# Performance work log

Hardware: AMD Instinct MI355X
Metric: run time of the kernel (lower is better)

The kernel has to match this reference:

```python
import jax, jax.numpy as jnp
import numpy as np

N_NODES = 100000
N_EDGES = 1600000
IN_FEATS, HID_FEATS, OUT_FEATS = 64, 64, 32


def setup_inputs() -> dict:
    key = jax.random.key(0)
    ks = jax.random.split(key, 8)
    x = jax.random.normal(ks[0], (N_NODES, IN_FEATS), dtype=jnp.float32)
    edge_index = jax.random.randint(ks[1], (2, N_EDGES), 0, N_NODES, dtype=jnp.int64)
    s1 = 1.0 / np.sqrt(IN_FEATS)
    s2 = 1.0 / np.sqrt(HID_FEATS)
    return {
        "x": x,
        "edge_index": edge_index,
        "W1l": jax.random.uniform(ks[2], (IN_FEATS, HID_FEATS), jnp.float32, -s1, s1),
        "W1r": jax.random.uniform(ks[3], (IN_FEATS, HID_FEATS), jnp.float32, -s1, s1),
        "b1": jnp.zeros((HID_FEATS,), jnp.float32),
        "W2l": jax.random.uniform(ks[4], (HID_FEATS, OUT_FEATS), jnp.float32, -s2, s2),
        "W2r": jax.random.uniform(ks[5], (HID_FEATS, OUT_FEATS), jnp.float32, -s2, s2),
        "b2": jnp.zeros((OUT_FEATS,), jnp.float32),
    }


def _mean_aggregate(h, src, dst, n_nodes):
    # gather source features, scatter-mean into destination nodes
    msg_sum = jax.ops.segment_sum(h[src], dst, num_segments=n_nodes)  # [N, D]
    cnt = jax.ops.segment_sum(jnp.ones(src.shape, h.dtype), dst, num_segments=n_nodes)
    return msg_sum / jnp.maximum(cnt, 1.0)[:, None]  # zero in-degree -> 0


def _sage_conv(h, src, dst, Wl, Wr, b):
    # PyG SAGEConv: lin_l(mean_j x_j) + lin_r(x_i); bias lives in lin_l
    agg = _mean_aggregate(h, src, dst, h.shape[0])
    return agg @ Wl + h @ Wr + b


def reference(x, edge_index, W1l, W1r, b1, W2l, W2r, b2):
    src, dst = edge_index[0], edge_index[1]
    h = jax.nn.relu(_sage_conv(x, src, dst, W1l, W1r, b1))
    out = _sage_conv(h, src, dst, W2l, W2r, b2)
    return out
```

## Files before the change

### kernel.cpp

```cpp
#include <hip/hip_runtime.h>

#define NN 100000
#define NE 1600000
#define NBK 392
#define CAPB 6144
#define CVTB 6250
#define EPA 2048

typedef __attribute__((ext_vector_type(8))) short bf16x8;
typedef __attribute__((ext_vector_type(4))) float f32x4;

__device__ __forceinline__ unsigned short f2b(float f) {
  unsigned b = __float_as_uint(f);
  unsigned r = b + 0x7FFF + ((b >> 16) & 1);
  return (unsigned short)(r >> 16);
}

__global__ void k_cvtpre(const float* __restrict__ x, unsigned short* __restrict__ xb,
                         const float* __restrict__ W1l, const float* __restrict__ W1r,
                         unsigned short* __restrict__ WT1,
                         const float* __restrict__ W2l, const float* __restrict__ W2r,
                         unsigned short* __restrict__ WT2, int* __restrict__ gcur) {
  int t = threadIdx.x;
  int b = blockIdx.x;
  if (b < CVTB) {
    int i = (b * 256 + t) * 4;
    float4 v = *(const float4*)(x + i);
    ushort4 o;
    o.x = f2b(v.x); o.y = f2b(v.y); o.z = f2b(v.z); o.w = f2b(v.w);
    *(ushort4*)(xb + i) = o;
    return;
  }
  if (b == CVTB) {
    for (int i = t; i < NBK; i += 256) gcur[i] = 0;
    for (int i = t; i < 64 * 128; i += 256) {
      int f = i >> 7, k = i & 127;
      WT1[i] = f2b((k < 64) ? W1l[k * 64 + f] : W1r[(k - 64) * 64 + f]);
    }
    return;
  }
  for (int i = t; i < 32 * 128; i += 256) {
    int f = i >> 7, k = i & 127;
    WT2[i] = f2b((k < 64) ? W2l[k * 32 + f] : W2r[(k - 64) * 32 + f]);
  }
}

__global__ void k_partA(const int* __restrict__ src, const int* __restrict__ dst,
                        int* __restrict__ gcur, unsigned* __restrict__ pairbuf) {
  __shared__ int hist[NBK];
  __shared__ int sc[512];
  __shared__ int base[NBK], lofs[NBK];
  __shared__ unsigned epk[EPA];
  __shared__ unsigned short ebk[EPA];
  int t = threadIdx.x;
  int pb = blockIdx.x;
  for (int i = t; i < NBK; i += 256) { hist[i] = 0; lofs[i] = 0; }
  __syncthreads();
  unsigned pk[EPA / 256]; int bk[EPA / 256];
  int e0 = pb * EPA + t;
#pragma unroll
  for (int j = 0; j < EPA / 256; ++j) {
    int e = e0 + j * 256;
    if (e < NE) {
      int d = dst[e], s = src[e];
      bk[j] = d >> 8;
      pk[j] = ((unsigned)s << 8) | (unsigned)(d & 255);
      atomicAdd(&hist[bk[j]], 1);
    } else bk[j] = -1;
  }
  __syncthreads();
  sc[t] = (t < NBK) ? hist[t] : 0;
  sc[t + 256] = (t + 256 < NBK) ? hist[t + 256] : 0;
  __syncthreads();
  for (int off = 1; off < 512; off <<= 1) {
    int v0 = (t >= off) ? sc[t - off] : 0;
    int v1 = sc[t + 256 - off];
    __syncthreads();
    sc[t] += v0;
    sc[t + 256] += v1;
    __syncthreads();
  }
  for (int i = t; i < NBK; i += 256) {
    int h = hist[i];
    base[i] = atomicAdd(&gcur[i], h);
    hist[i] = sc[i] - h;
  }
  __syncthreads();
#pragma unroll
  for (int j = 0; j < EPA / 256; ++j) {
    if (bk[j] >= 0) {
      int pos = hist[bk[j]] + atomicAdd(&lofs[bk[j]], 1);
      epk[pos] = pk[j];
      ebk[pos] = (unsigned short)bk[j];
    }
  }
  __syncthreads();
  int cb = sc[511];
  for (int i = t; i < cb; i += 256) {
    unsigned p = epk[i];
    int bb = ebk[i];
    int slot = base[bb] + (i - hist[bb]);
    if (slot < CAPB) pairbuf[(size_t)bb * CAPB + slot] = p;
  }
}

__global__ void k_partB(const unsigned* __restrict__ pairbuf, const int* __restrict__ gcur,
                        int* __restrict__ esrc, uint2* __restrict__ rowp2) {
  __shared__ int cnt[256], cur[256], ssum[256];
  __shared__ int ebuf[CAPB];
  int b = blockIdx.x, t = threadIdx.x;
  int cb = gcur[b]; if (cb > CAPB) cb = CAPB;
  if (t < 256) cnt[t] = 0;
  __syncthreads();
  const unsigned* pb = pairbuf + (size_t)b * CAPB;
  for (int i = t; i < cb; i += 512) atomicAdd(&cnt[pb[i] & 255], 1);
  __syncthreads();
  int a0 = (t < 256) ? cnt[t] : 0;
  if (t < 256) ssum[t] = a0;
  __syncthreads();
  for (int off = 1; off < 256; off <<= 1) {
    int tmp = (t < 256 && t >= off) ? ssum[t - off] : 0;
    __syncthreads();
    if (t < 256) ssum[t] += tmp;
    __syncthreads();
  }
  if (t < 256) {
    int ex = ssum[t] - a0;
    cur[t] = ex;
    int n = b * 256 + t;
    if (n < NN) rowp2[n] = make_uint2((unsigned)(b * CAPB + ex),
                                      (unsigned)(b * CAPB + ex + a0));
  }
  __syncthreads();
  for (int i = t; i < cb; i += 512) {
    unsigned p = pb[i];
    int pos = atomicAdd(&cur[p & 255], 1);
    ebuf[pos] = (int)(p >> 8);
  }
  __syncthreads();
  for (int i = t; i < cb; i += 512) esrc[(size_t)b * CAPB + i] = ebuf[i];
}

__global__ void k_agg(const uint2* __restrict__ fb64, const uint2* __restrict__ rowp2,
                      const int* __restrict__ esrc, uint2* __restrict__ aggb64) {
  int tid = blockIdx.x * 256 + threadIdx.x;
  int node = tid >> 4;
  int c16 = tid & 15;
  int qbase = (threadIdx.x & 63) & 48;
  uint2 rp = rowp2[node];
  int beg = (int)rp.x, deg = (int)(rp.y - rp.x);
  float a0 = 0.f, a1 = 0.f, a2 = 0.f, a3 = 0.f;

  for (int r0 = 0; r0 < deg; r0 += 16) {
    int rem = deg - r0; if (rem > 16) rem = 16;
    int idxv = esrc[beg + r0 + (c16 < rem ? c16 : 0)];
    int sv[16];
#pragma unroll
    for (int j = 0; j < 16; ++j) sv[j] = __shfl(idxv, qbase + j);
    uint2 v[16];
#pragma unroll
    for (int j = 0; j < 16; ++j)
      if (j < rem) v[j] = fb64[(size_t)sv[j] * 16 + c16];
    __builtin_amdgcn_sched_barrier(0);
#pragma unroll
    for (int j = 0; j < 16; ++j)
      if (j < rem) {
        a0 += __uint_as_float(v[j].x << 16);
        a1 += __uint_as_float(v[j].x & 0xFFFF0000u);
        a2 += __uint_as_float(v[j].y << 16);
        a3 += __uint_as_float(v[j].y & 0xFFFF0000u);
      }
  }
  float inv = (deg > 0) ? (1.0f / (float)deg) : 0.f;
  uint2 o;
  o.x = (unsigned)f2b(a0 * inv) | ((unsigned)f2b(a1 * inv) << 16);
  o.y = (unsigned)f2b(a2 * inv) | ((unsigned)f2b(a3 * inv) << 16);
  aggb64[(size_t)node * 16 + c16] = o;
}

template <int NF>
__global__ __launch_bounds__(256) void k_gemm(
    const unsigned short* __restrict__ aggb, const unsigned short* __restrict__ featb,
    const unsigned short* __restrict__ WT, const float* __restrict__ bias,
    float* __restrict__ out, unsigned short* __restrict__ ob, int relu) {
  __shared__ unsigned short As[64 * 128];
  __shared__ unsigned short Ws[NF * 128];
  int tid = threadIdx.x;
  int n0 = blockIdx.x * 64;
  int lane = tid & 63, wr = tid >> 6;

  for (int cch = tid; cch < 64 * 16; cch += 256) {
    int r = cch >> 4, s = cch & 15;
    int n = n0 + r;
    bf16x8 v = {0, 0, 0, 0, 0, 0, 0, 0};
    if (n < NN) {
      const unsigned short* p = (s < 8) ? (aggb + (size_t)n * 64 + s * 8)
                                        : (featb + (size_t)n * 64 + (s - 8) * 8);
      v = *(const bf16x8*)p;
    }
    *(bf16x8*)(&As[r * 128 + ((s ^ (r & 15)) << 3)]) = v;
  }
  for (int cch = tid; cch < NF * 16; cch += 256) {
    int f = cch >> 4, s = cch & 15;
    bf16x8 v = *(const bf16x8*)(WT + f * 128 + s * 8);
    *(bf16x8*)(&Ws[f * 128 + ((s ^ (f & 15)) << 3)]) = v;
  }
  __syncthreads();

  int l15 = lane & 15, lg = lane >> 4;
  int arow = wr * 16 + l15;
  f32x4 acc[NF / 16];
#pragma unroll
  for (int ct = 0; ct < NF / 16; ++ct) acc[ct] = (f32x4){0.f, 0.f, 0.f, 0.f};

#pragma unroll
  for (int k0 = 0; k0 < 4; ++k0) {
    int sa = k0 * 4 + lg;
    bf16x8 a = *(const bf16x8*)(&As[arow * 128 + ((sa ^ (arow & 15)) << 3)]);
#pragma unroll
    for (int ct = 0; ct < NF / 16; ++ct) {
      int bcol = ct * 16 + l15;
      bf16x8 b = *(const bf16x8*)(&Ws[bcol * 128 + ((sa ^ (bcol & 15)) << 3)]);
      acc[ct] = __builtin_amdgcn_mfma_f32_16x16x32_bf16(a, b, acc[ct], 0, 0, 0);
    }
  }

#pragma unroll
  for (int ct = 0; ct < NF / 16; ++ct) {
    int f = ct * 16 + l15;
    float bv = bias[f];
#pragma unroll
    for (int r = 0; r < 4; ++r) {
      int n = n0 + wr * 16 + lg * 4 + r;
      if (n >= NN) continue;
      float v = acc[ct][r] + bv;
      if (relu) v = fmaxf(v, 0.f);
      if (out) out[(size_t)n * NF + f] = v;
      if (ob) ob[(size_t)n * NF + f] = f2b(v);
    }
  }
}

extern "C" void kernel_launch(void* const* d_in, const int* in_sizes, int n_in,
                              void* d_out, int out_size, void* d_ws, size_t ws_size,
                              hipStream_t stream) {
  const float* x   = (const float*)d_in[0];
  const int*   ei  = (const int*)d_in[1];
  const float* W1l = (const float*)d_in[2];
  const float* W1r = (const float*)d_in[3];
  const float* b1  = (const float*)d_in[4];
  const float* W2l = (const float*)d_in[5];
  const float* W2r = (const float*)d_in[6];
  const float* b2  = (const float*)d_in[7];
  const int* src = ei;
  const int* dst = ei + NE;
  float* out = (float*)d_out;

  char* ws = (char*)d_ws;
  size_t off = 0;
  auto take = [&](size_t bytes) -> char* {
    char* p = ws + off;
    off = (off + bytes + 255) & ~(size_t)255;
    return p;
  };
  int*      gcur    = (int*)take((size_t)NBK * 4);
  unsigned* pairbuf = (unsigned*)take((size_t)NBK * CAPB * 4);
  int*      esrc    = (int*)take((size_t)NBK * CAPB * 4);
  uint2*    rowp2   = (uint2*)take((size_t)NN * 8);
  unsigned short* aggb = (unsigned short*)take((size_t)NN * 64 * 2);
  unsigned short* xb   = (unsigned short*)take((size_t)NN * 64 * 2);
  unsigned short* hb   = (unsigned short*)take((size_t)NN * 64 * 2);
  unsigned short* WT1  = (unsigned short*)take((size_t)64 * 128 * 2);
  unsigned short* WT2  = (unsigned short*)take((size_t)32 * 128 * 2);

  int nbA = (NE + EPA - 1) / EPA;
  k_cvtpre<<<CVTB + 2, 256, 0, stream>>>(x, xb, W1l, W1r, WT1, W2l, W2r, WT2, gcur);
  k_partA<<<nbA, 256, 0, stream>>>(src, dst, gcur, pairbuf);
  k_partB<<<NBK, 512, 0, stream>>>(pairbuf, gcur, esrc, rowp2);

  int nbG = (NN + 63) / 64;
  k_agg<<<NN / 16, 256, 0, stream>>>((const uint2*)xb, rowp2, esrc, (uint2*)aggb);
  k_gemm<64><<<nbG, 256, 0, stream>>>(aggb, xb, WT1, b1, nullptr, hb, 1);
  k_agg<<<NN / 16, 256, 0, stream>>>((const uint2*)hb, rowp2, esrc, (uint2*)aggb);
  k_gemm<32><<<nbG, 256, 0, stream>>>(aggb, hb, WT2, b2, out, nullptr, 0);
}
```

Measured before the change: 133.8 us.

## Fuse mean aggregation into GEMM kernels and merge conversion with partition pass

The neighbour gather and mean aggregation now run inside the GEMM kernel. Each block aggregates its 64 nodes straight into shared memory, so the bf16 aggregate buffer no longer makes a round trip through global memory. The bf16 conversion and weight-transpose blocks are merged into the edge-partition kernel, with a tiny separate kernel zeroing the bucket counters, which cuts the launch count from 7 to 5. The trade-off is that each fused block processes 64 nodes in sequence with less parallelism per launch, and the larger merged kernel may lower occupancy because of its shared-memory footprint.

Measured after the change: 134.6 us. No clear change (+0.7%).

```diff
diff --git a/kernel.cpp b/kernel.cpp
--- a/kernel.cpp
+++ b/kernel.cpp
@@ -16,11 +16,22 @@
   return (unsigned short)(r >> 16);
 }
 
-__global__ void k_cvtpre(const float* __restrict__ x, unsigned short* __restrict__ xb,
-                         const float* __restrict__ W1l, const float* __restrict__ W1r,
-                         unsigned short* __restrict__ WT1,
-                         const float* __restrict__ W2l, const float* __restrict__ W2r,
-                         unsigned short* __restrict__ WT2, int* __restrict__ gcur) {
+__global__ void k_zero(int* __restrict__ g) {
+  if (threadIdx.x < NBK) g[threadIdx.x] = 0;
+}
+
+__global__ void k_pre(const float* __restrict__ x, unsigned short* __restrict__ xb,
+                      const float* __restrict__ W1l, const float* __restrict__ W1r,
+                      unsigned short* __restrict__ WT1,
+                      const float* __restrict__ W2l, const float* __restrict__ W2r,
+                      unsigned short* __restrict__ WT2,
+                      const int* __restrict__ src, const int* __restrict__ dst,
+                      int* __restrict__ gcur, unsigned* __restrict__ pairbuf) {
+  __shared__ int hist[NBK];
+  __shared__ int sc[512];
+  __shared__ int base[NBK], lofs[NBK];
+  __shared__ unsigned epk[EPA];
+  __shared__ unsigned short ebk[EPA];
   int t = threadIdx.x;
   int b = blockIdx.x;
   if (b < CVTB) {
@@ -32,28 +43,20 @@
     return;
   }
   if (b == CVTB) {
-    for (int i = t; i < NBK; i += 256) gcur[i] = 0;
     for (int i = t; i < 64 * 128; i += 256) {
       int f = i >> 7, k = i & 127;
       WT1[i] = f2b((k < 64) ? W1l[k * 64 + f] : W1r[(k - 64) * 64 + f]);
     }
     return;
   }
-  for (int i = t; i < 32 * 128; i += 256) {
-    int f = i >> 7, k = i & 127;
-    WT2[i] = f2b((k < 64) ? W2l[k * 32 + f] : W2r[(k - 64) * 32 + f]);
-  }
-}
-
-__global__ void k_partA(const int* __restrict__ src, const int* __restrict__ dst,
-                        int* __restrict__ gcur, unsigned* __restrict__ pairbuf) {
-  __shared__ int hist[NBK];
-  __shared__ int sc[512];
-  __shared__ int base[NBK], lofs[NBK];
-  __shared__ unsigned epk[EPA];
-  __shared__ unsigned short ebk[EPA];
-  int t = threadIdx.x;
-  int pb = blockIdx.x;
+  if (b == CVTB + 1) {
+    for (int i = t; i < 32 * 128; i += 256) {
+      int f = i >> 7, k = i & 127;
+      WT2[i] = f2b((k < 64) ? W2l[k * 32 + f] : W2r[(k - 64) * 32 + f]);
+    }
+    return;
+  }
+  int pb = b - (CVTB + 2);
   for (int i = t; i < NBK; i += 256) { hist[i] = 0; lofs[i] = 0; }
   __syncthreads();
   unsigned pk[EPA / 256]; int bk[EPA / 256];
@@ -141,78 +144,80 @@
   for (int i = t; i < cb; i += 512) esrc[(size_t)b * CAPB + i] = ebuf[i];
 }
 
-__global__ void k_agg(const uint2* __restrict__ fb64, const uint2* __restrict__ rowp2,
-                      const int* __restrict__ esrc, uint2* __restrict__ aggb64) {
-  int tid = blockIdx.x * 256 + threadIdx.x;
-  int node = tid >> 4;
-  int c16 = tid & 15;
-  int qbase = (threadIdx.x & 63) & 48;
-  uint2 rp = rowp2[node];
-  int beg = (int)rp.x, deg = (int)(rp.y - rp.x);
-  float a0 = 0.f, a1 = 0.f, a2 = 0.f, a3 = 0.f;
-
-  for (int r0 = 0; r0 < deg; r0 += 16) {
-    int rem = deg - r0; if (rem > 16) rem = 16;
-    int idxv = esrc[beg + r0 + (c16 < rem ? c16 : 0)];
-    int sv[16];
-#pragma unroll
-    for (int j = 0; j < 16; ++j) sv[j] = __shfl(idxv, qbase + j);
-    uint2 v[16];
-#pragma unroll
-    for (int j = 0; j < 16; ++j)
-      if (j < rem) v[j] = fb64[(size_t)sv[j] * 16 + c16];
-    __builtin_amdgcn_sched_barrier(0);
-#pragma unroll
-    for (int j = 0; j < 16; ++j)
-      if (j < rem) {
-        a0 += __uint_as_float(v[j].x << 16);
-        a1 += __uint_as_float(v[j].x & 0xFFFF0000u);
-        a2 += __uint_as_float(v[j].y << 16);
-        a3 += __uint_as_float(v[j].y & 0xFFFF0000u);
-      }
-  }
-  float inv = (deg > 0) ? (1.0f / (float)deg) : 0.f;
-  uint2 o;
-  o.x = (unsigned)f2b(a0 * inv) | ((unsigned)f2b(a1 * inv) << 16);
-  o.y = (unsigned)f2b(a2 * inv) | ((unsigned)f2b(a3 * inv) << 16);
-  aggb64[(size_t)node * 16 + c16] = o;
-}
-
 template <int NF>
-__global__ __launch_bounds__(256) void k_gemm(
-    const unsigned short* __restrict__ aggb, const unsigned short* __restrict__ featb,
+__global__ __launch_bounds__(256) void k_agemm(
+    const unsigned short* __restrict__ featb,
+    const uint2* __restrict__ rowp2, const int* __restrict__ esrc,
     const unsigned short* __restrict__ WT, const float* __restrict__ bias,
     float* __restrict__ out, unsigned short* __restrict__ ob, int relu) {
   __shared__ unsigned short As[64 * 128];
   __shared__ unsigned short Ws[NF * 128];
   int tid = threadIdx.x;
   int n0 = blockIdx.x * 64;
-  int lane = tid & 63, wr = tid >> 6;
-
-  for (int cch = tid; cch < 64 * 16; cch += 256) {
-    int r = cch >> 4, s = cch & 15;
-    int n = n0 + r;
-    bf16x8 v = {0, 0, 0, 0, 0, 0, 0, 0};
-    if (n < NN) {
-      const unsigned short* p = (s < 8) ? (aggb + (size_t)n * 64 + s * 8)
-                                        : (featb + (size_t)n * 64 + (s - 8) * 8);
-      v = *(const bf16x8*)p;
-    }
-    *(bf16x8*)(&As[r * 128 + ((s ^ (r & 15)) << 3)]) = v;
-  }
+
   for (int cch = tid; cch < NF * 16; cch += 256) {
     int f = cch >> 4, s = cch & 15;
     bf16x8 v = *(const bf16x8*)(WT + f * 128 + s * 8);
     *(bf16x8*)(&Ws[f * 128 + ((s ^ (f & 15)) << 3)]) = v;
   }
-  __syncthreads();
-
+  for (int cch = tid; cch < 64 * 8; cch += 256) {
+    int r = cch >> 3, s8 = cch & 7;
+    int s = s8 + 8;
+    int n = n0 + r;
+    bf16x8 v = {0, 0, 0, 0, 0, 0, 0, 0};
+    if (n < NN) v = *(const bf16x8*)(featb + (size_t)n * 64 + s8 * 8);
+    *(bf16x8*)(&As[r * 128 + ((s ^ (r & 15)) << 3)]) = v;
+  }
+
+  const uint2* fb64 = (const uint2*)featb;
+  int c16 = tid & 15;
+  int qid = tid >> 4;
+  int qbase = tid & 48;
+#pragma unroll
+  for (int nd = 0; nd < 4; ++nd) {
+    int r = qid + nd * 16;
+    int node = n0 + r;
+    int beg = 0, deg = 0;
+    if (node < NN) {
+      uint2 rp = rowp2[node];
+      beg = (int)rp.x; deg = (int)(rp.y - rp.x);
+    }
+    float a0 = 0.f, a1 = 0.f, a2 = 0.f, a3 = 0.f;
+    for (int r0 = 0; r0 < deg; r0 += 16) {
+      int rem = deg - r0; if (rem > 16) rem = 16;
+      int idxv = esrc[beg + r0 + (c16 < rem ? c16 : 0)];
+      int sv[16];
+#pragma unroll
+      for (int j = 0; j < 16; ++j) sv[j] = __shfl(idxv, qbase + j);
+      uint2 v[16];
+#pragma unroll
+      for (int j = 0; j < 16; ++j)
+        if (j < rem) v[j] = fb64[(size_t)sv[j] * 16 + c16];
+      __builtin_amdgcn_sched_barrier(0);
+#pragma unroll
+      for (int j = 0; j < 16; ++j)
+        if (j < rem) {
+          a0 += __uint_as_float(v[j].x << 16);
+          a1 += __uint_as_float(v[j].x & 0xFFFF0000u);
+          a2 += __uint_as_float(v[j].y << 16);
+          a3 += __uint_as_float(v[j].y & 0xFFFF0000u);
+        }
+    }
+    float inv = (deg > 0) ? (1.0f / (float)deg) : 0.f;
+    int s = c16 >> 1;
+    uint2 o;
+    o.x = (unsigned)f2b(a0 * inv) | ((unsigned)f2b(a1 * inv) << 16);
+    o.y = (unsigned)f2b(a2 * inv) | ((unsigned)f2b(a3 * inv) << 16);
+    *(uint2*)(&As[r * 128 + ((s ^ (r & 15)) << 3) + (c16 & 1) * 4]) = o;
+  }
+  __syncthreads();
+
+  int lane = tid & 63, wr = tid >> 6;
   int l15 = lane & 15, lg = lane >> 4;
   int arow = wr * 16 + l15;
   f32x4 acc[NF / 16];
 #pragma unroll
   for (int ct = 0; ct < NF / 16; ++ct) acc[ct] = (f32x4){0.f, 0.f, 0.f, 0.f};
-
 #pragma unroll
   for (int k0 = 0; k0 < 4; ++k0) {
     int sa = k0 * 4 + lg;
@@ -267,20 +272,19 @@
   unsigned* pairbuf = (unsigned*)take((size_t)NBK * CAPB * 4);
   int*      esrc    = (int*)take((size_t)NBK * CAPB * 4);
   uint2*    rowp2   = (uint2*)take((size_t)NN * 8);
-  unsigned short* aggb = (unsigned short*)take((size_t)NN * 64 * 2);
-  unsigned short* xb   = (unsigned short*)take((size_t)NN * 64 * 2);
-  unsigned short* hb   = (unsigned short*)take((size_t)NN * 64 * 2);
-  unsigned short* WT1  = (unsigned short*)take((size_t)64 * 128 * 2);
-  unsigned short* WT2  = (unsigned short*)take((size_t)32 * 128 * 2);
+  unsigned short* xb  = (unsigned short*)take((size_t)NN * 64 * 2);
+  unsigned short* hb  = (unsigned short*)take((size_t)NN * 64 * 2);
+  unsigned short* WT1 = (unsigned short*)take((size_t)64 * 128 * 2);
+  unsigned short* WT2 = (unsigned short*)take((size_t)32 * 128 * 2);
 
   int nbA = (NE + EPA - 1) / EPA;
-  k_cvtpre<<<CVTB + 2, 256, 0, stream>>>(x, xb, W1l, W1r, WT1, W2l, W2r, WT2, gcur);
-  k_partA<<<nbA, 256, 0, stream>>>(src, dst, gcur, pairbuf);
+  int nbG = (NN + 63) / 64;
+
+  k_zero<<<1, 512, 0, stream>>>(gcur);
+  k_pre<<<CVTB + 2 + nbA, 256, 0, stream>>>(x, xb, W1l, W1r, WT1, W2l, W2r, WT2,
+                                            src, dst, gcur, pairbuf);
   k_partB<<<NBK, 512, 0, stream>>>(pairbuf, gcur, esrc, rowp2);
 
-  int nbG = (NN + 63) / 64;
-  k_agg<<<NN / 16, 256, 0, stream>>>((const uint2*)xb, rowp2, esrc, (uint2*)aggb);
-  k_gemm<64><<<nbG, 256, 0, stream>>>(aggb, xb, WT1, b1, nullptr, hb, 1);
-  k_agg<<<NN / 16, 256, 0, stream>>>((const uint2*)hb, rowp2, esrc, (uint2*)aggb);
-  k_gemm<32><<<nbG, 256, 0, stream>>>(aggb, hb, WT2, b2, out, nullptr, 0);
-}
+  k_agemm<64><<<nbG, 256, 0, stream>>>(xb, rowp2, esrc, WT1, b1, nullptr, hb, 1);
+  k_agemm<32><<<nbG, 256, 0, stream>>>(hb, rowp2, esrc, WT2, b2, out, nullptr, 0);
+}
```
